# Kernel tuning notes

Measured on AMD Instinct MI355X. Metric: run time of the kernel, lower is better.

## Reference

```python
import jax, jax.numpy as jnp
import numpy as np

B, N, M, D, H, DFF = 1, 2048, 2048, 1024, 16, 4096
MASK_VAL = -50000.0
EPS = 1e-5


def _xavier(k, shape):
    lim = np.sqrt(6.0 / (shape[0] + shape[1])).astype(np.float32)
    return jax.random.uniform(k, shape, jnp.float32, -lim, lim)


def setup_inputs() -> dict:
    key = jax.random.key(0)
    ks = jax.random.split(key, 8)
    return {
        "x": jax.random.normal(ks[0], (B, N, D), jnp.float32),
        "context": jax.random.normal(ks[1], (B, M, D), jnp.float32),
        "Wq": _xavier(ks[2], (D, D)), "bq": jnp.zeros((D,), jnp.float32),
        "Wkv": _xavier(ks[3], (D, 2 * D)), "bkv": jnp.zeros((2 * D,), jnp.float32),
        "Wo": _xavier(ks[4], (D, D)), "bo": jnp.zeros((D,), jnp.float32),
        "ln1_g": jnp.ones((D,), jnp.float32), "ln1_b": jnp.zeros((D,), jnp.float32),
        "W1": _xavier(ks[5], (D, DFF)), "bf1": jnp.zeros((DFF,), jnp.float32),
        "W2": _xavier(ks[6], (DFF, D)), "bf2": jnp.zeros((D,), jnp.float32),
        "ln2_g": jnp.ones((D,), jnp.float32), "ln2_b": jnp.zeros((D,), jnp.float32),
    }


def _layernorm(x, g, b):
    mu = x.mean(-1, keepdims=True)
    var = ((x - mu) ** 2).mean(-1, keepdims=True)
    return (x - mu) * jax.lax.rsqrt(var + EPS) * g + b


def reference(x, context, Wq, bq, Wkv, bkv, Wo, bo, ln1_g, ln1_b, W1, bf1, W2, bf2, ln2_g, ln2_b):
    b, n, d = x.shape
    m = context.shape[1]
    h = H
    dh = d // h
    scale = dh ** -0.5
    # q from x only; k,v from [x; context]
    q = (x @ Wq + bq).reshape(b, n, h, dh).transpose(0, 2, 1, 3)          # b h n dh
    kv_in = jnp.concatenate([x, context], axis=1)                          # b (n+m) d
    k, v = jnp.split(kv_in @ Wkv + bkv, 2, axis=-1)
    k = k.reshape(b, n + m, h, dh).transpose(0, 2, 1, 3)                   # b h (n+m) dh
    v = v.reshape(b, n + m, h, dh).transpose(0, 2, 1, 3)
    dots = jnp.einsum('bhid,bhjd->bhij', q * scale, k)                     # b h n (n+m)
    # causal mask applies only to the self-attention (first n) key columns
    rows = jnp.arange(n)[:, None]
    cols = jnp.arange(n + m)[None, :]
    causal = (cols < n) & (cols > rows)
    dots = jnp.where(causal, MASK_VAL, dots)
    attn = jax.nn.softmax(dots, axis=-1)                                   # dropout = identity (eval)
    out = jnp.einsum('bhij,bhjd->bhid', attn, v)
    out = out.transpose(0, 2, 1, 3).reshape(b, n, d) @ Wo + bo
    # PostNorm(Residual(attn))
    x1 = _layernorm(x + out, ln1_g, ln1_b)
    # PostNorm(Residual(FFN)) with exact-erf GELU
    ff = jax.nn.gelu(x1 @ W1 + bf1, approximate=False) @ W2 + bf2
    return _layernorm(x1 + ff, ln2_g, ln2_b)
```

## Files before the change

kernel.cpp:

```cpp
#include <hip/hip_runtime.h>


using bf16x8 = __attribute__((ext_vector_type(8))) short;
using f32x4  = __attribute__((ext_vector_type(4))) float;

__device__ __forceinline__ ushort f2bf(float f) {
    unsigned u = __float_as_uint(f);
    unsigned r = (u + 0x7fffu + ((u >> 16) & 1u)) >> 16;
    return (ushort)r;
}

__device__ __forceinline__ void gload16(const void* g, void* l) {
    __builtin_amdgcn_global_load_lds(
        (const __attribute__((address_space(1))) void*)g,
        (__attribute__((address_space(3))) void*)l, 16, 0, 0);
}

__device__ __forceinline__ float gelu_erf(float v) {
    return 0.5f * v * (1.0f + erff(v * 0.70710678118654752f));
}

__device__ __forceinline__ uint cvtpk(float a, float b) {
    uint r;
    asm("v_cvt_pk_bf16_f32 %0, %1, %2" : "=v"(r) : "v"(a), "v"(b));
    return r;
}

__global__ __launch_bounds__(256) void cvt4(const float* __restrict__ in,
                                            ushort* __restrict__ out, int n) {
    int i = (blockIdx.x * 256 + threadIdx.x) * 4;
    if (i + 3 < n) {
        float4 v = *(const float4*)(in + i);
        ushort4 o;
        o.x = f2bf(v.x); o.y = f2bf(v.y); o.z = f2bf(v.z); o.w = f2bf(v.w);
        *(ushort4*)(out + i) = o;
    }
}

__global__ __launch_bounds__(256) void tcvt(const float* __restrict__ in,
                                            ushort* __restrict__ out, int R, int C) {
    __shared__ float tile[32][33];
    const int tx = threadIdx.x, ty = threadIdx.y;
    const int c0 = blockIdx.x * 32, r0 = blockIdx.y * 32;
#pragma unroll
    for (int i = 0; i < 4; ++i)
        tile[ty + 8 * i][tx] = in[(size_t)(r0 + ty + 8 * i) * C + c0 + tx];
    __syncthreads();
#pragma unroll
    for (int i = 0; i < 4; ++i)
        out[(size_t)(c0 + ty + 8 * i) * R + r0 + tx] = f2bf(tile[tx][ty + 8 * i]);
}

__global__ __launch_bounds__(256) void vtrans(const ushort* __restrict__ KV,
                                              ushort* __restrict__ Vt) {
    __shared__ ushort tile[32][34];
    const int tx = threadIdx.x, ty = threadIdx.y;
    const int j0 = blockIdx.x * 32, d0 = blockIdx.y * 32;
#pragma unroll
    for (int i = 0; i < 4; ++i)
        tile[ty + 8 * i][tx] = KV[(size_t)(j0 + ty + 8 * i) * 2048 + 1024 + d0 + tx];
    __syncthreads();
#pragma unroll
    for (int i = 0; i < 4; ++i)
        Vt[(size_t)(d0 + ty + 8 * i) * 4096 + j0 + tx] = tile[tx][ty + 8 * i];
}

template <int BM, int BN, int ACT, int OUTF32, int RES, int SCALED, int SPLITK>
__global__ __launch_bounds__(256) void gemm_bt(
    const ushort* __restrict__ A, int lda, const ushort* __restrict__ Bt, int ldb,
    const float* __restrict__ bias, const float* __restrict__ resid,
    void* __restrict__ Cout, int M, int N, int K, float scale) {
    constexpr int MR = BM / 32, NR = BN / 32;
    __shared__ __align__(16) ushort Asm[BM * 64];
    __shared__ __align__(16) ushort Bsm[BN * 64];
    const int tid = threadIdx.x;
    const int w = tid >> 6, lane = tid & 63, g = lane >> 4, i15 = lane & 15;
    const int wm = w >> 1, wn = w & 1;
    const int m0 = blockIdx.y * BM, n0 = blockIdx.x * BN;
    if (SPLITK) {
        A += (size_t)blockIdx.z * K;
        Bt += (size_t)blockIdx.z * K;
    }

    f32x4 acc[MR][NR] = {};

    for (int kt = 0; kt < K; kt += 64) {
#pragma unroll
        for (int q = 0; q < BM / 32; ++q) {
            int off = (w * (BM / 32) + q) * 1024 + lane * 16;
            int r = off >> 7, cb = off & 127;
            int scb = cb ^ ((r & 7) << 4);
            const void* src = (const char*)A + ((size_t)(m0 + r) * lda + kt) * 2 + scb;
            gload16(src, (char*)Asm + (w * (BM / 32) + q) * 1024);
        }
#pragma unroll
        for (int q = 0; q < BN / 32; ++q) {
            int off = (w * (BN / 32) + q) * 1024 + lane * 16;
            int r = off >> 7, cb = off & 127;
            int scb = cb ^ ((r & 7) << 4);
            const void* src = (const char*)Bt + ((size_t)(n0 + r) * ldb + kt) * 2 + scb;
            gload16(src, (char*)Bsm + (w * (BN / 32) + q) * 1024);
        }
        __syncthreads();

#pragma unroll
        for (int kc = 0; kc < 2; ++kc) {
            bf16x8 af[MR], bfr[NR];
#pragma unroll
            for (int mi = 0; mi < MR; ++mi) {
                int r = wm * (BM / 2) + mi * 16 + i15;
                af[mi] = *(const bf16x8*)((const char*)Asm + r * 128 +
                                          ((kc * 64 + g * 16) ^ ((r & 7) << 4)));
            }
#pragma unroll
            for (int ni = 0; ni < NR; ++ni) {
                int r = wn * (BN / 2) + ni * 16 + i15;
                bfr[ni] = *(const bf16x8*)((const char*)Bsm + r * 128 +
                                           ((kc * 64 + g * 16) ^ ((r & 7) << 4)));
            }
#pragma unroll
            for (int mi = 0; mi < MR; ++mi)
#pragma unroll
                for (int ni = 0; ni < NR; ++ni)
                    acc[mi][ni] = __builtin_amdgcn_mfma_f32_16x16x32_bf16(
                        af[mi], bfr[ni], acc[mi][ni], 0, 0, 0);
        }
        __syncthreads();
    }

    float* Cf = (float*)Cout;
    if (SPLITK) Cf += (size_t)blockIdx.z * M * N;

#pragma unroll
    for (int ni = 0; ni < NR; ++ni) {
        int col = n0 + wn * (BN / 2) + ni * 16 + i15;
        float bb = bias ? bias[col] : 0.f;
#pragma unroll
        for (int mi = 0; mi < MR; ++mi) {
#pragma unroll
            for (int r2 = 0; r2 < 4; ++r2) {
                int row = m0 + wm * (BM / 2) + mi * 16 + 4 * g + r2;
                float v = acc[mi][ni][r2] + bb;
                if (ACT) v = gelu_erf(v);
                if (SCALED) v *= scale;
                size_t off = (size_t)row * N + col;
                if (OUTF32) {
                    float rv = RES ? resid[off] : 0.f;
                    Cf[off] = v + rv;
                } else {
                    ((ushort*)Cout)[off] = f2bf(v);
                }
            }
        }
    }
}

template <int NS>
__global__ __launch_bounds__(512) void flash_attn(
    const ushort* __restrict__ Q,
    const ushort* __restrict__ KVb,
    const ushort* __restrict__ Vt,
    ushort* __restrict__ O,
    float* __restrict__ Opart,
    float* __restrict__ Ml) {
    constexpr int D = 1024;
    __shared__ __align__(16) ushort Ksm[2][64 * 64];
    __shared__ __align__(16) ushort Vsm[2][64 * 64];
    __shared__ __align__(16) ushort Psm[8][16 * 64];

    const int tid = threadIdx.x;
    const int w = tid >> 6, lane = tid & 63, g = lane >> 4, i15 = lane & 15;
    const int bid = blockIdx.x;
    const int h = bid & 15;
    const int qB = 15 - ((bid >> 4) & 15);
    const int s = (NS > 1) ? (bid >> 8) : 0;
    const int qb = qB * 128 + w * 16;
    const int qrow = qb + i15;
    const int diagW = qb >> 6;
    const int diagB = 2 * qB + 1;
    const int nt = diagB + 33;
    const int lo = (s * nt) / NS;
    const int hi = ((s + 1) * nt) / NS;

    bf16x8 qf[2];
    qf[0] = *(const bf16x8*)(Q + (size_t)qrow * D + h * 64 + g * 8);
    qf[1] = *(const bf16x8*)(Q + (size_t)qrow * D + h * 64 + 32 + g * 8);

    f32x4 o[4] = {};
    float m_run = -INFINITY, l_run = 0.f;

    const int sr  = tid >> 3;
    const int scb = (tid & 7) * 16;
    const int ssw = scb ^ ((sr & 7) << 4);
    const char* kb0 = (const char*)KVb + ((size_t)sr * 2048 + h * 64) * 2 + scb;
    const char* vb0 = (const char*)Vt + ((size_t)(h * 64 + sr) * 4096) * 2 + scb;

    uint4 kreg, vreg;
    auto jt_of = [&](int t) { return (t <= diagB) ? t : (32 + (t - diagB - 1)); };
    auto stage = [&](int t) {
        const int jt = jt_of(t);
        kreg = *(const uint4*)(kb0 + (size_t)jt * 64 * 4096);
        vreg = *(const uint4*)(vb0 + (size_t)jt * 128);
    };
    auto wlds = [&](int buf) {
        *(uint4*)((char*)Ksm[buf] + sr * 128 + ssw) = kreg;
        *(uint4*)((char*)Vsm[buf] + sr * 128 + ssw) = vreg;
    };

    const int pbase = i15 * 128;
    const int psw = (i15 & 7) << 4;

    auto body = [&](int buf, int t) {
        const int jt = jt_of(t);
        f32x4 st[4];
#pragma unroll
        for (int jg = 0; jg < 4; ++jg) {
            int jr = jg * 16 + i15;
            bf16x8 ka0 = *(const bf16x8*)((const char*)Ksm[buf] + jr * 128 +
                                          ((g * 16) ^ ((jr & 7) << 4)));
            bf16x8 ka1 = *(const bf16x8*)((const char*)Ksm[buf] + jr * 128 +
                                          ((64 + g * 16) ^ ((jr & 7) << 4)));
            f32x4 z = {};
            z = __builtin_amdgcn_mfma_f32_16x16x32_bf16(ka0, qf[0], z, 0, 0, 0);
            z = __builtin_amdgcn_mfma_f32_16x16x32_bf16(ka1, qf[1], z, 0, 0, 0);
            st[jg] = z;
        }
        if (jt >= diagW && jt <= diagB) {
#pragma unroll
            for (int jg = 0; jg < 4; ++jg)
#pragma unroll
                for (int r = 0; r < 4; ++r) {
                    int j = jt * 64 + jg * 16 + 4 * g + r;
                    if (j > qrow) st[jg][r] = -50000.f;
                }
        }

        float v8[8];
#pragma unroll
        for (int jg = 0; jg < 4; ++jg) {
            v8[2 * jg]     = fmaxf(st[jg][0], st[jg][1]);
            v8[2 * jg + 1] = fmaxf(st[jg][2], st[jg][3]);
        }
        v8[0] = fmaxf(v8[0], v8[4]); v8[1] = fmaxf(v8[1], v8[5]);
        v8[2] = fmaxf(v8[2], v8[6]); v8[3] = fmaxf(v8[3], v8[7]);
        float mt = fmaxf(fmaxf(v8[0], v8[1]), fmaxf(v8[2], v8[3]));
        mt = fmaxf(mt, __shfl_xor(mt, 16));
        mt = fmaxf(mt, __shfl_xor(mt, 32));

        const bool skip = __all(mt - m_run <= 8.f);
        float mnew, fscale;
        if (skip) { mnew = m_run; fscale = 1.f; }
        else      { mnew = fmaxf(m_run, mt); fscale = exp2f(m_run - mnew); }

        float pf[4][4], sj[4];
#pragma unroll
        for (int jg = 0; jg < 4; ++jg) {
#pragma unroll
            for (int r = 0; r < 4; ++r) pf[jg][r] = exp2f(st[jg][r] - mnew);
            sj[jg] = (pf[jg][0] + pf[jg][1]) + (pf[jg][2] + pf[jg][3]);
        }
        float psum = (sj[0] + sj[1]) + (sj[2] + sj[3]);
        psum += __shfl_xor(psum, 16);
        psum += __shfl_xor(psum, 32);
        l_run = l_run * fscale + psum;
        m_run = mnew;

        if (!skip) {
#pragma unroll
            for (int r = 0; r < 4; ++r) {
                float fr = __shfl(fscale, 20 * g + r);
#pragma unroll
                for (int dg = 0; dg < 4; ++dg) o[dg][r] *= fr;
            }
        }

#pragma unroll
        for (int jg = 0; jg < 4; ++jg) {
            uint2 pk;
            pk.x = cvtpk(pf[jg][0], pf[jg][1]);
            pk.y = cvtpk(pf[jg][2], pf[jg][3]);
            *(uint2*)((char*)Psm[w] + pbase + ((jg * 32 + g * 8) ^ psw)) = pk;
        }

#pragma unroll
        for (int jc = 0; jc < 2; ++jc) {
            bf16x8 pa = *(const bf16x8*)((const char*)Psm[w] + pbase +
                                         ((jc * 64 + g * 16) ^ psw));
#pragma unroll
            for (int dg = 0; dg < 4; ++dg) {
                int dr = dg * 16 + i15;
                bf16x8 vb = *(const bf16x8*)((const char*)Vsm[buf] + dr * 128 +
                                             ((jc * 64 + g * 16) ^ ((dr & 7) << 4)));
                o[dg] = __builtin_amdgcn_mfma_f32_16x16x32_bf16(pa, vb, o[dg], 0, 0, 0);
            }
        }
    };

    stage(lo);
    wlds(0);
    __syncthreads();

    int t = lo;
    for (; t + 1 < hi; t += 2) {
        stage(t + 1);
        body(0, t);
        wlds(1);
        __syncthreads();
        if (t + 2 < hi) stage(t + 2);
        body(1, t + 1);
        if (t + 2 < hi) { wlds(0); __syncthreads(); }
    }
    if (t < hi) body(0, t);

    if (NS > 1) {
        if (g == 0) {
            float* mp = Ml + ((size_t)(s * 2048 + qrow) * 16 + h) * 2;
            mp[0] = m_run; mp[1] = l_run;
        }
#pragma unroll
        for (int r = 0; r < 4; ++r)
#pragma unroll
            for (int dg = 0; dg < 4; ++dg) {
                int row = qb + 4 * g + r;
                int col = h * 64 + dg * 16 + i15;
                Opart[(size_t)(s * 2048 + row) * 1024 + col] = o[dg][r];
            }
    } else {
#pragma unroll
        for (int r = 0; r < 4; ++r) {
            float lr = __shfl(l_run, 20 * g + r);
            float inv = 1.f / lr;
#pragma unroll
            for (int dg = 0; dg < 4; ++dg) {
                int row = qb + 4 * g + r;
                int col = h * 64 + dg * 16 + i15;
                O[(size_t)row * D + col] = f2bf(o[dg][r] * inv);
            }
        }
    }
}

template <int NS>
__global__ __launch_bounds__(256) void attn_combine(
    const float* __restrict__ Opart, const float* __restrict__ Ml,
    ushort* __restrict__ O) {
    const int row = blockIdx.x, tid = threadIdx.x;
    const int c = tid * 4, h = c >> 6;
    float ms[NS], ls[NS];
#pragma unroll
    for (int s = 0; s < NS; ++s) {
        const float* mp = Ml + ((size_t)(s * 2048 + row) * 16 + h) * 2;
        ms[s] = mp[0]; ls[s] = mp[1];
    }
    float m = ms[0];
#pragma unroll
    for (int s = 1; s < NS; ++s) m = fmaxf(m, ms[s]);
    float denom = 0.f, wgt[NS];
#pragma unroll
    for (int s = 0; s < NS; ++s) { wgt[s] = exp2f(ms[s] - m); denom += ls[s] * wgt[s]; }
    const float inv = 1.f / denom;
    float ax = 0, ay = 0, az = 0, aw = 0;
#pragma unroll
    for (int s = 0; s < NS; ++s) {
        float4 a = *(const float4*)(Opart + (size_t)(s * 2048 + row) * 1024 + c);
        ax += a.x * wgt[s]; ay += a.y * wgt[s]; az += a.z * wgt[s]; aw += a.w * wgt[s];
    }
    ushort4 ob;
    ob.x = f2bf(ax * inv); ob.y = f2bf(ay * inv);
    ob.z = f2bf(az * inv); ob.w = f2bf(aw * inv);
    *(ushort4*)(O + (size_t)row * 1024 + c) = ob;
}

__global__ __launch_bounds__(256) void layernorm_k(
    const float* __restrict__ in, const float* __restrict__ gam,
    const float* __restrict__ bet, float* __restrict__ outf,
    ushort* __restrict__ outb) {
    const int row = blockIdx.x, tid = threadIdx.x;
    const float4 v = *(const float4*)(in + (size_t)row * 1024 + tid * 4);
    float s = v.x + v.y + v.z + v.w;
    float sq = v.x * v.x + v.y * v.y + v.z * v.z + v.w * v.w;
#pragma unroll
    for (int d = 1; d < 64; d <<= 1) {
        s += __shfl_xor(s, d);
        sq += __shfl_xor(sq, d);
    }
    __shared__ float red[8];
    const int w = tid >> 6;
    if ((tid & 63) == 0) { red[w] = s; red[4 + w] = sq; }
    __syncthreads();
    s = red[0] + red[1] + red[2] + red[3];
    sq = red[4] + red[5] + red[6] + red[7];
    const float mu = s * (1.f / 1024.f);
    const float rs = rsqrtf(sq * (1.f / 1024.f) - mu * mu + 1e-5f);
    const float4 gg = *(const float4*)(gam + tid * 4);
    const float4 bb = *(const float4*)(bet + tid * 4);
    float4 o;
    o.x = (v.x - mu) * rs * gg.x + bb.x;
    o.y = (v.y - mu) * rs * gg.y + bb.y;
    o.z = (v.z - mu) * rs * gg.z + bb.z;
    o.w = (v.w - mu) * rs * gg.w + bb.w;
    *(float4*)(outf + (size_t)row * 1024 + tid * 4) = o;
    if (outb) {
        ushort4 ob;
        ob.x = f2bf(o.x); ob.y = f2bf(o.y); ob.z = f2bf(o.z); ob.w = f2bf(o.w);
        *(ushort4*)(outb + (size_t)row * 1024 + tid * 4) = ob;
    }
}

template <int NP>
__global__ __launch_bounds__(256) void layernorm_comb(
    const float* __restrict__ P,
    const float* __restrict__ bias, const float* __restrict__ resid,
    const float* __restrict__ gam, const float* __restrict__ bet,
    float* __restrict__ outf) {
    const int row = blockIdx.x, tid = threadIdx.x;
    const float4 rr = *(const float4*)(resid + (size_t)row * 1024 + tid * 4);
    const float4 bs = *(const float4*)(bias + tid * 4);
    float4 v;
    v.x = rr.x + bs.x; v.y = rr.y + bs.y; v.z = rr.z + bs.z; v.w = rr.w + bs.w;
#pragma unroll
    for (int p = 0; p < NP; ++p) {
        const float4 a = *(const float4*)(P + (size_t)(p * 2048 + row) * 1024 + tid * 4);
        v.x += a.x; v.y += a.y; v.z += a.z; v.w += a.w;
    }
    float s = v.x + v.y + v.z + v.w;
    float sq = v.x * v.x + v.y * v.y + v.z * v.z + v.w * v.w;
#pragma unroll
    for (int d = 1; d < 64; d <<= 1) {
        s += __shfl_xor(s, d);
        sq += __shfl_xor(sq, d);
    }
    __shared__ float red[8];
    const int w = tid >> 6;
    if ((tid & 63) == 0) { red[w] = s; red[4 + w] = sq; }
    __syncthreads();
    s = red[0] + red[1] + red[2] + red[3];
    sq = red[4] + red[5] + red[6] + red[7];
    const float mu = s * (1.f / 1024.f);
    const float rs = rsqrtf(sq * (1.f / 1024.f) - mu * mu + 1e-5f);
    const float4 gg = *(const float4*)(gam + tid * 4);
    const float4 bb = *(const float4*)(bet + tid * 4);
    float4 o;
    o.x = (v.x - mu) * rs * gg.x + bb.x;
    o.y = (v.y - mu) * rs * gg.y + bb.y;
    o.z = (v.z - mu) * rs * gg.z + bb.z;
    o.w = (v.w - mu) * rs * gg.w + bb.w;
    *(float4*)(outf + (size_t)row * 1024 + tid * 4) = o;
}

extern "C" void kernel_launch(void* const* d_in, const int* in_sizes, int n_in,
                              void* d_out, int out_size, void* d_ws, size_t ws_size,
                              hipStream_t stream) {
    const float* x    = (const float*)d_in[0];
    const float* ctx  = (const float*)d_in[1];
    const float* Wq   = (const float*)d_in[2];
    const float* bq   = (const float*)d_in[3];
    const float* Wkv  = (const float*)d_in[4];
    const float* bkv  = (const float*)d_in[5];
    const float* Wo   = (const float*)d_in[6];
    const float* bo   = (const float*)d_in[7];
    const float* g1   = (const float*)d_in[8];
    const float* b1   = (const float*)d_in[9];
    const float* W1   = (const float*)d_in[10];
    const float* bf1  = (const float*)d_in[11];
    const float* W2   = (const float*)d_in[12];
    const float* bf2  = (const float*)d_in[13];
    const float* g2   = (const float*)d_in[14];
    const float* b2   = (const float*)d_in[15];

    char* ws = (char*)d_ws;
    const size_t MB = 1u << 20;
    ushort* XCb  = (ushort*)(ws + 0);
    ushort* WoT  = (ushort*)(ws + 8 * MB);
    ushort* W1T  = (ushort*)(ws + 10 * MB);
    ushort* W2T  = (ushort*)(ws + 18 * MB);
    ushort* WqT  = (ushort*)(ws + 26 * MB);
    ushort* WkvT = (ushort*)(ws + 28 * MB);
    ushort* Qs   = (ushort*)(ws + 32 * MB);
    ushort* attn = (ushort*)(ws + 36 * MB);
    ushort* KV   = (ushort*)(ws + 40 * MB);
    ushort* Vt   = (ushort*)(ws + 56 * MB);
    ushort* x1b  = (ushort*)(ws + 26 * MB);
    float*  x1f  = (float*)(ws + 32 * MB);
    ushort* ffb  = (ushort*)(ws + 40 * MB);
    float*  y1   = (float*)(ws + 56 * MB);
    float*  Opart = (float*)(ws + 64 * MB);
    float*  Pk4   = (float*)(ws + 64 * MB);
    float*  Pk2   = (float*)(ws + 0);

    cvt4<<<2048, 256, 0, stream>>>(x, XCb, 2048 * 1024);
    cvt4<<<2048, 256, 0, stream>>>(ctx, XCb + 2048 * 1024, 2048 * 1024);
    tcvt<<<dim3(32, 32), dim3(32, 8), 0, stream>>>(Wq, WqT, 1024, 1024);
    tcvt<<<dim3(64, 32), dim3(32, 8), 0, stream>>>(Wkv, WkvT, 1024, 2048);
    tcvt<<<dim3(32, 32), dim3(32, 8), 0, stream>>>(Wo, WoT, 1024, 1024);
    tcvt<<<dim3(128, 32), dim3(32, 8), 0, stream>>>(W1, W1T, 1024, 4096);
    tcvt<<<dim3(32, 128), dim3(32, 8), 0, stream>>>(W2, W2T, 4096, 1024);
    gemm_bt<64, 128, 0, 0, 0, 1, 0><<<dim3(8, 32), 256, 0, stream>>>(
        XCb, 1024, WqT, 1024, bq, nullptr, Qs, 2048, 1024, 1024, 0.18033688011112042f);
    gemm_bt<128, 128, 0, 0, 0, 0, 0><<<dim3(16, 32), 256, 0, stream>>>(
        XCb, 1024, WkvT, 1024, bkv, nullptr, KV, 4096, 2048, 1024, 1.f);
    vtrans<<<dim3(128, 32), dim3(32, 8), 0, stream>>>(KV, Vt);

    if (ws_size >= 97 * MB) {
        float* Ml = (float*)(ws + 96 * MB);
        flash_attn<4><<<1024, 512, 0, stream>>>(Qs, KV, Vt, nullptr, Opart, Ml);
        attn_combine<4><<<2048, 256, 0, stream>>>(Opart, Ml, attn);
    } else if (ws_size >= 81 * MB) {
        float* Ml = (float*)(ws + 80 * MB);
        flash_attn<2><<<512, 512, 0, stream>>>(Qs, KV, Vt, nullptr, Opart, Ml);
        attn_combine<2><<<2048, 256, 0, stream>>>(Opart, Ml, attn);
    } else {
        flash_attn<1><<<256, 512, 0, stream>>>(Qs, KV, Vt, attn, nullptr, nullptr);
    }

    gemm_bt<64, 128, 0, 1, 1, 0, 0><<<dim3(8, 32), 256, 0, stream>>>(
        attn, 1024, WoT, 1024, bo, x, y1, 2048, 1024, 1024, 1.f);
    layernorm_k<<<2048, 256, 0, stream>>>(y1, g1, b1, x1f, x1b);
    gemm_bt<128, 128, 1, 0, 0, 0, 0><<<dim3(32, 16), 256, 0, stream>>>(
        x1b, 1024, W1T, 1024, bf1, nullptr, ffb, 2048, 4096, 1024, 1.f);
    if (ws_size >= 96 * MB) {
        gemm_bt<128, 128, 0, 1, 0, 0, 1><<<dim3(8, 16, 4), 256, 0, stream>>>(
            ffb, 4096, W2T, 4096, nullptr, nullptr, Pk4, 2048, 1024, 1024, 1.f);
        layernorm_comb<4><<<2048, 256, 0, stream>>>(Pk4, bf2, x1f, g2, b2,
                                                    (float*)d_out);
    } else {
        gemm_bt<128, 128, 0, 1, 0, 0, 1><<<dim3(8, 16, 2), 256, 0, stream>>>(
            ffb, 4096, W2T, 4096, nullptr, nullptr, Pk2, 2048, 1024, 2048, 1.f);
        layernorm_comb<2><<<2048, 256, 0, stream>>>(Pk2, bf2, x1f, g2, b2,
                                                    (float*)d_out);
    }
}
```

Before: 234.1 us.

## Fuse V transpose into KV GEMM, batch weight conversions, store bf16 partials

The KV projection GEMM now writes K into its own buffer and writes V already transposed, which removes the separate vtrans kernel and the extra pass over V. The five weight transpose-convert launches are merged into one kernel that dispatches on block index. Flash-attention split partials are stored as bf16 instead of fp32, halving combine traffic at some precision cost. s_setprio hints are added around the MFMA sections, and workspace offsets are reshuffled so the split-4 path fits in less memory.

```diff
diff --git a/kernel.cpp b/kernel.cpp
--- a/kernel.cpp
+++ b/kernel.cpp
@@ -10,6 +10,10 @@
     return (ushort)r;
 }
 
+__device__ __forceinline__ float bf2f(ushort u) {
+    return __uint_as_float((uint)u << 16);
+}
+
 __device__ __forceinline__ void gload16(const void* g, void* l) {
     __builtin_amdgcn_global_load_lds(
         (const __attribute__((address_space(1))) void*)g,
@@ -26,10 +30,10 @@
     return r;
 }
 
-__global__ __launch_bounds__(256) void cvt4(const float* __restrict__ in,
-                                            ushort* __restrict__ out, int n) {
-    int i = (blockIdx.x * 256 + threadIdx.x) * 4;
-    if (i + 3 < n) {
+__global__ __launch_bounds__(256) void cvt_all(const float* __restrict__ in,
+                                               ushort* __restrict__ out, int n) {
+    for (int i = (blockIdx.x * 256 + threadIdx.x) * 4; i + 3 < n;
+         i += gridDim.x * 1024) {
         float4 v = *(const float4*)(in + i);
         ushort4 o;
         o.x = f2bf(v.x); o.y = f2bf(v.y); o.z = f2bf(v.z); o.w = f2bf(v.w);
@@ -37,11 +41,24 @@
     }
 }
 
-__global__ __launch_bounds__(256) void tcvt(const float* __restrict__ in,
-                                            ushort* __restrict__ out, int R, int C) {
+__global__ __launch_bounds__(256) void tcvt_all(
+    const float* __restrict__ Wq, const float* __restrict__ Wkv,
+    const float* __restrict__ Wo, const float* __restrict__ W1,
+    const float* __restrict__ W2,
+    ushort* __restrict__ WqT, ushort* __restrict__ WkvT,
+    ushort* __restrict__ WoT, ushort* __restrict__ W1T,
+    ushort* __restrict__ W2T) {
     __shared__ float tile[32][33];
-    const int tx = threadIdx.x, ty = threadIdx.y;
-    const int c0 = blockIdx.x * 32, r0 = blockIdx.y * 32;
+    int b = blockIdx.x;
+    const float* in; ushort* out; int R, C, loc;
+    if (b < 1024)      { in = Wq;  out = WqT;  R = 1024; C = 1024; loc = b; }
+    else if (b < 3072) { in = Wkv; out = WkvT; R = 1024; C = 2048; loc = b - 1024; }
+    else if (b < 4096) { in = Wo;  out = WoT;  R = 1024; C = 1024; loc = b - 3072; }
+    else if (b < 8192) { in = W1;  out = W1T;  R = 1024; C = 4096; loc = b - 4096; }
+    else               { in = W2;  out = W2T;  R = 4096; C = 1024; loc = b - 8192; }
+    const int nbx = C >> 5;
+    const int c0 = (loc % nbx) * 32, r0 = (loc / nbx) * 32;
+    const int tx = threadIdx.x & 31, ty = threadIdx.x >> 5;
 #pragma unroll
     for (int i = 0; i < 4; ++i)
         tile[ty + 8 * i][tx] = in[(size_t)(r0 + ty + 8 * i) * C + c0 + tx];
@@ -51,25 +68,12 @@
         out[(size_t)(c0 + ty + 8 * i) * R + r0 + tx] = f2bf(tile[tx][ty + 8 * i]);
 }
 
-__global__ __launch_bounds__(256) void vtrans(const ushort* __restrict__ KV,
-                                              ushort* __restrict__ Vt) {
-    __shared__ ushort tile[32][34];
-    const int tx = threadIdx.x, ty = threadIdx.y;
-    const int j0 = blockIdx.x * 32, d0 = blockIdx.y * 32;
-#pragma unroll
-    for (int i = 0; i < 4; ++i)
-        tile[ty + 8 * i][tx] = KV[(size_t)(j0 + ty + 8 * i) * 2048 + 1024 + d0 + tx];
-    __syncthreads();
-#pragma unroll
-    for (int i = 0; i < 4; ++i)
-        Vt[(size_t)(d0 + ty + 8 * i) * 4096 + j0 + tx] = tile[tx][ty + 8 * i];
-}
-
-template <int BM, int BN, int ACT, int OUTF32, int RES, int SCALED, int SPLITK>
+template <int BM, int BN, int ACT, int OUTF32, int RES, int SCALED, int SPLITK, int VT>
 __global__ __launch_bounds__(256) void gemm_bt(
     const ushort* __restrict__ A, int lda, const ushort* __restrict__ Bt, int ldb,
     const float* __restrict__ bias, const float* __restrict__ resid,
-    void* __restrict__ Cout, int M, int N, int K, float scale) {
+    void* __restrict__ Cout, ushort* __restrict__ Vout,
+    int M, int N, int K, float scale) {
     constexpr int MR = BM / 32, NR = BN / 32;
     __shared__ __align__(16) ushort Asm[BM * 64];
     __shared__ __align__(16) ushort Bsm[BN * 64];
@@ -137,18 +141,29 @@
         float bb = bias ? bias[col] : 0.f;
 #pragma unroll
         for (int mi = 0; mi < MR; ++mi) {
-#pragma unroll
-            for (int r2 = 0; r2 < 4; ++r2) {
-                int row = m0 + wm * (BM / 2) + mi * 16 + 4 * g + r2;
-                float v = acc[mi][ni][r2] + bb;
-                if (ACT) v = gelu_erf(v);
-                if (SCALED) v *= scale;
-                size_t off = (size_t)row * N + col;
-                if (OUTF32) {
-                    float rv = RES ? resid[off] : 0.f;
-                    Cf[off] = v + rv;
-                } else {
-                    ((ushort*)Cout)[off] = f2bf(v);
+            if (VT && col >= 1024) {
+                int row = m0 + wm * (BM / 2) + mi * 16 + 4 * g;
+                ushort4 ov;
+                ov.x = f2bf(acc[mi][ni][0] + bb);
+                ov.y = f2bf(acc[mi][ni][1] + bb);
+                ov.z = f2bf(acc[mi][ni][2] + bb);
+                ov.w = f2bf(acc[mi][ni][3] + bb);
+                *(ushort4*)(Vout + (size_t)(col - 1024) * 4096 + row) = ov;
+            } else {
+#pragma unroll
+                for (int r2 = 0; r2 < 4; ++r2) {
+                    int row = m0 + wm * (BM / 2) + mi * 16 + 4 * g + r2;
+                    float v = acc[mi][ni][r2] + bb;
+                    if (ACT) v = gelu_erf(v);
+                    if (SCALED) v *= scale;
+                    size_t off = VT ? ((size_t)row * 1024 + col)
+                                    : ((size_t)row * N + col);
+                    if (OUTF32) {
+                        float rv = RES ? resid[off] : 0.f;
+                        Cf[off] = v + rv;
+                    } else {
+                        ((ushort*)Cout)[off] = f2bf(v);
+                    }
                 }
             }
         }
@@ -158,10 +173,10 @@
 template <int NS>
 __global__ __launch_bounds__(512) void flash_attn(
     const ushort* __restrict__ Q,
-    const ushort* __restrict__ KVb,
+    const ushort* __restrict__ Kb,
     const ushort* __restrict__ Vt,
     ushort* __restrict__ O,
-    float* __restrict__ Opart,
+    ushort* __restrict__ Opart,
     float* __restrict__ Ml) {
     constexpr int D = 1024;
     __shared__ __align__(16) ushort Ksm[2][64 * 64];
@@ -192,14 +207,14 @@
     const int sr  = tid >> 3;
     const int scb = (tid & 7) * 16;
     const int ssw = scb ^ ((sr & 7) << 4);
-    const char* kb0 = (const char*)KVb + ((size_t)sr * 2048 + h * 64) * 2 + scb;
+    const char* kb0 = (const char*)Kb + ((size_t)sr * 1024 + h * 64) * 2 + scb;
     const char* vb0 = (const char*)Vt + ((size_t)(h * 64 + sr) * 4096) * 2 + scb;
 
     uint4 kreg, vreg;
     auto jt_of = [&](int t) { return (t <= diagB) ? t : (32 + (t - diagB - 1)); };
     auto stage = [&](int t) {
         const int jt = jt_of(t);
-        kreg = *(const uint4*)(kb0 + (size_t)jt * 64 * 4096);
+        kreg = *(const uint4*)(kb0 + (size_t)jt * 64 * 2048);
         vreg = *(const uint4*)(vb0 + (size_t)jt * 128);
     };
     auto wlds = [&](int buf) {
@@ -213,6 +228,7 @@
     auto body = [&](int buf, int t) {
         const int jt = jt_of(t);
         f32x4 st[4];
+        __builtin_amdgcn_s_setprio(1);
 #pragma unroll
         for (int jg = 0; jg < 4; ++jg) {
             int jr = jg * 16 + i15;
@@ -225,6 +241,7 @@
             z = __builtin_amdgcn_mfma_f32_16x16x32_bf16(ka1, qf[1], z, 0, 0, 0);
             st[jg] = z;
         }
+        __builtin_amdgcn_s_setprio(0);
         if (jt >= diagW && jt <= diagB) {
 #pragma unroll
             for (int jg = 0; jg < 4; ++jg)
@@ -282,6 +299,7 @@
             *(uint2*)((char*)Psm[w] + pbase + ((jg * 32 + g * 8) ^ psw)) = pk;
         }
 
+        __builtin_amdgcn_s_setprio(1);
 #pragma unroll
         for (int jc = 0; jc < 2; ++jc) {
             bf16x8 pa = *(const bf16x8*)((const char*)Psm[w] + pbase +
@@ -294,6 +312,7 @@
                 o[dg] = __builtin_amdgcn_mfma_f32_16x16x32_bf16(pa, vb, o[dg], 0, 0, 0);
             }
         }
+        __builtin_amdgcn_s_setprio(0);
     };
 
     stage(lo);
@@ -323,7 +342,7 @@
             for (int dg = 0; dg < 4; ++dg) {
                 int row = qb + 4 * g + r;
                 int col = h * 64 + dg * 16 + i15;
-                Opart[(size_t)(s * 2048 + row) * 1024 + col] = o[dg][r];
+                Opart[(size_t)(s * 2048 + row) * 1024 + col] = f2bf(o[dg][r]);
             }
     } else {
 #pragma unroll
@@ -342,7 +361,7 @@
 
 template <int NS>
 __global__ __launch_bounds__(256) void attn_combine(
-    const float* __restrict__ Opart, const float* __restrict__ Ml,
+    const ushort* __restrict__ Opart, const float* __restrict__ Ml,
     ushort* __restrict__ O) {
     const int row = blockIdx.x, tid = threadIdx.x;
     const int c = tid * 4, h = c >> 6;
@@ -362,8 +381,9 @@
     float ax = 0, ay = 0, az = 0, aw = 0;
 #pragma unroll
     for (int s = 0; s < NS; ++s) {
-        float4 a = *(const float4*)(Opart + (size_t)(s * 2048 + row) * 1024 + c);
-        ax += a.x * wgt[s]; ay += a.y * wgt[s]; az += a.z * wgt[s]; aw += a.w * wgt[s];
+        ushort4 a = *(const ushort4*)(Opart + (size_t)(s * 2048 + row) * 1024 + c);
+        ax += bf2f(a.x) * wgt[s]; ay += bf2f(a.y) * wgt[s];
+        az += bf2f(a.z) * wgt[s]; aw += bf2f(a.w) * wgt[s];
     }
     ushort4 ob;
     ob.x = f2bf(ax * inv); ob.y = f2bf(ay * inv);
@@ -478,54 +498,54 @@
     ushort* WkvT = (ushort*)(ws + 28 * MB);
     ushort* Qs   = (ushort*)(ws + 32 * MB);
     ushort* attn = (ushort*)(ws + 36 * MB);
-    ushort* KV   = (ushort*)(ws + 40 * MB);
-    ushort* Vt   = (ushort*)(ws + 56 * MB);
+    ushort* Kb   = (ushort*)(ws + 40 * MB);
+    ushort* Vt   = (ushort*)(ws + 48 * MB);
     ushort* x1b  = (ushort*)(ws + 26 * MB);
     float*  x1f  = (float*)(ws + 32 * MB);
     ushort* ffb  = (ushort*)(ws + 40 * MB);
     float*  y1   = (float*)(ws + 56 * MB);
-    float*  Opart = (float*)(ws + 64 * MB);
+    ushort* Opart = (ushort*)(ws + 64 * MB);
     float*  Pk4   = (float*)(ws + 64 * MB);
     float*  Pk2   = (float*)(ws + 0);
 
-    cvt4<<<2048, 256, 0, stream>>>(x, XCb, 2048 * 1024);
-    cvt4<<<2048, 256, 0, stream>>>(ctx, XCb + 2048 * 1024, 2048 * 1024);
-    tcvt<<<dim3(32, 32), dim3(32, 8), 0, stream>>>(Wq, WqT, 1024, 1024);
-    tcvt<<<dim3(64, 32), dim3(32, 8), 0, stream>>>(Wkv, WkvT, 1024, 2048);
-    tcvt<<<dim3(32, 32), dim3(32, 8), 0, stream>>>(Wo, WoT, 1024, 1024);
-    tcvt<<<dim3(128, 32), dim3(32, 8), 0, stream>>>(W1, W1T, 1024, 4096);
-    tcvt<<<dim3(32, 128), dim3(32, 8), 0, stream>>>(W2, W2T, 4096, 1024);
-    gemm_bt<64, 128, 0, 0, 0, 1, 0><<<dim3(8, 32), 256, 0, stream>>>(
-        XCb, 1024, WqT, 1024, bq, nullptr, Qs, 2048, 1024, 1024, 0.18033688011112042f);
-    gemm_bt<128, 128, 0, 0, 0, 0, 0><<<dim3(16, 32), 256, 0, stream>>>(
-        XCb, 1024, WkvT, 1024, bkv, nullptr, KV, 4096, 2048, 1024, 1.f);
-    vtrans<<<dim3(128, 32), dim3(32, 8), 0, stream>>>(KV, Vt);
-
-    if (ws_size >= 97 * MB) {
-        float* Ml = (float*)(ws + 96 * MB);
-        flash_attn<4><<<1024, 512, 0, stream>>>(Qs, KV, Vt, nullptr, Opart, Ml);
+    cvt_all<<<2048, 256, 0, stream>>>(x, XCb, 2048 * 1024);
+    cvt_all<<<2048, 256, 0, stream>>>(ctx, XCb + 2048 * 1024, 2048 * 1024);
+    tcvt_all<<<12288, 256, 0, stream>>>(Wq, Wkv, Wo, W1, W2,
+                                        WqT, WkvT, WoT, W1T, W2T);
+    gemm_bt<64, 128, 0, 0, 0, 1, 0, 0><<<dim3(8, 32), 256, 0, stream>>>(
+        XCb, 1024, WqT, 1024, bq, nullptr, Qs, nullptr,
+        2048, 1024, 1024, 0.18033688011112042f);
+    gemm_bt<128, 128, 0, 0, 0, 0, 0, 1><<<dim3(16, 32), 256, 0, stream>>>(
+        XCb, 1024, WkvT, 1024, bkv, nullptr, Kb, Vt,
+        4096, 2048, 1024, 1.f);
+
+    if (ws_size >= 82 * MB) {
+        float* Ml = (float*)(ws + 80 * MB);
+        flash_attn<4><<<1024, 512, 0, stream>>>(Qs, Kb, Vt, nullptr, Opart, Ml);
         attn_combine<4><<<2048, 256, 0, stream>>>(Opart, Ml, attn);
-    } else if (ws_size >= 81 * MB) {
-        float* Ml = (float*)(ws + 80 * MB);
-        flash_attn<2><<<512, 512, 0, stream>>>(Qs, KV, Vt, nullptr, Opart, Ml);
+    } else if (ws_size >= 73 * MB) {
+        float* Ml = (float*)(ws + 72 * MB);
+        flash_attn<2><<<512, 512, 0, stream>>>(Qs, Kb, Vt, nullptr, Opart, Ml);
         attn_combine<2><<<2048, 256, 0, stream>>>(Opart, Ml, attn);
     } else {
-        flash_attn<1><<<256, 512, 0, stream>>>(Qs, KV, Vt, attn, nullptr, nullptr);
-    }
-
-    gemm_bt<64, 128, 0, 1, 1, 0, 0><<<dim3(8, 32), 256, 0, stream>>>(
-        attn, 1024, WoT, 1024, bo, x, y1, 2048, 1024, 1024, 1.f);
+        flash_attn<1><<<256, 512, 0, stream>>>(Qs, Kb, Vt, attn, nullptr, nullptr);
+    }
+
+    gemm_bt<64, 128, 0, 1, 1, 0, 0, 0><<<dim3(8, 32), 256, 0, stream>>>(
+        attn, 1024, WoT, 1024, bo, x, y1, nullptr, 2048, 1024, 1024, 1.f);
     layernorm_k<<<2048, 256, 0, stream>>>(y1, g1, b1, x1f, x1b);
-    gemm_bt<128, 128, 1, 0, 0, 0, 0><<<dim3(32, 16), 256, 0, stream>>>(
-        x1b, 1024, W1T, 1024, bf1, nullptr, ffb, 2048, 4096, 1024, 1.f);
+    gemm_bt<128, 128, 1, 0, 0, 0, 0, 0><<<dim3(32, 16), 256, 0, stream>>>(
+        x1b, 1024, W1T, 1024, bf1, nullptr, ffb, nullptr, 2048, 4096, 1024, 1.f);
     if (ws_size >= 96 * MB) {
-        gemm_bt<128, 128, 0, 1, 0, 0, 1><<<dim3(8, 16, 4), 256, 0, stream>>>(
-            ffb, 4096, W2T, 4096, nullptr, nullptr, Pk4, 2048, 1024, 1024, 1.f);
+        gemm_bt<128, 128, 0, 1, 0, 0, 1, 0><<<dim3(8, 16, 4), 256, 0, stream>>>(
+            ffb, 4096, W2T, 4096, nullptr, nullptr, Pk4, nullptr,
+            2048, 1024, 1024, 1.f);
         layernorm_comb<4><<<2048, 256, 0, stream>>>(Pk4, bf2, x1f, g2, b2,
                                                     (float*)d_out);
     } else {
-        gemm_bt<128, 128, 0, 1, 0, 0, 1><<<dim3(8, 16, 2), 256, 0, stream>>>(
-            ffb, 4096, W2T, 4096, nullptr, nullptr, Pk2, 2048, 1024, 2048, 1.f);
+        gemm_bt<128, 128, 0, 1, 0, 0, 1, 0><<<dim3(8, 16, 2), 256, 0, stream>>>(
+            ffb, 4096, W2T, 4096, nullptr, nullptr, Pk2, nullptr,
+            2048, 1024, 2048, 1.f);
         layernorm_comb<2><<<2048, 256, 0, stream>>>(Pk2, bf2, x1f, g2, b2,
                                                     (float*)d_out);
     }
```

After: 222.7 us. 4.9% less time.
